# Kernel tuning notes

Hardware: AMD Instinct MI355X
Metric: run time of the kernel (lower is better)

Reference implementation:

```python
import jax, jax.numpy as jnp
import numpy as np

P = 16            # patch_size
D = 256           # hidden_dim == P*P (required by final reshape)
H = 8             # num_heads
HD = D // H       # head_dim


def _sinusoid(n, d):
    # standard sinusoidal positional encoding, interleaved sin/cos
    pos = jnp.arange(n, dtype=jnp.float32)[:, None]            # (n,1)
    i = jnp.arange(0, d, 2, dtype=jnp.float32)                 # (d/2,)
    div = jnp.exp(-i * (jnp.log(10000.0) / d))                 # (d/2,)
    ang = pos * div                                            # (n, d/2)
    return jnp.stack([jnp.sin(ang), jnp.cos(ang)], axis=-1).reshape(n, d)


def _patch_embed(x, w, b):
    # Conv2d(in_ch, D, kernel=P, stride=P) then flatten to (B, N, D)
    e = jax.lax.conv_general_dilated(
        x, w, window_strides=(P, P), padding='VALID',
        dimension_numbers=('NCHW', 'OIHW', 'NCHW'))
    e = e + b[None, :, None, None]
    B = e.shape[0]
    e = e.reshape(B, D, -1).transpose(0, 2, 1)                 # (B, N, D)
    e = e + _sinusoid(e.shape[1], D)[None]                     # positional enc
    return e.reshape(B, -1, H, HD).transpose(0, 2, 1, 3)       # (B, H, N, HD)


def setup_inputs() -> dict:
    key = jax.random.key(0)
    ks = jax.random.split(key, 12)
    B = 16
    inp = {
        'q': jax.random.normal(ks[0], (B, 3, 512, 512), jnp.float32),
        'k': jax.random.normal(ks[1], (B, 3, 512, 512), jnp.float32),
        'v': jax.random.normal(ks[2], (B, 3, 512, 512), jnp.float32),
        'a': jax.random.normal(ks[3], (B, 3, 256, 256), jnp.float32),
    }
    s = 0.02
    for idx, name in enumerate('qkva'):
        inp['w' + name] = jax.random.normal(ks[4 + 2 * idx], (D, 3, P, P), jnp.float32) * s
        inp['b' + name] = jnp.zeros((D,), jnp.float32)
    return inp


def reference(q, k, v, a, wq, bq, wk, bk, wv, bv, wa, ba):
    qh = _patch_embed(q, wq, bq)   # (B,H,Nq,HD), Nq=1024
    kh = _patch_embed(k, wk, bk)   # (B,H,Nk,HD)
    vh = _patch_embed(v, wv, bv)   # (B,H,Nk,HD)
    ah = _patch_embed(a, wa, ba)   # (B,H,Na,HD), Na=256
    scale = HD ** -0.5
    # agent attention: two small softmax matmuls then Q @ (K @ V)
    Qs = jax.nn.softmax(jnp.einsum('bhnd,bhmd->bhnm', qh, ah) * scale, axis=-1)  # (B,H,Nq,Na)
    Ks = jax.nn.softmax(jnp.einsum('bhmd,bhnd->bhmn', ah, kh) * scale, axis=-1)  # (B,H,Na,Nk)
    KV = jnp.einsum('bhmn,bhnd->bhmd', Ks, vh)                                   # (B,H,Na,HD)
    A = jnp.einsum('bhnm,bhmd->bhnd', Qs, KV)                                    # (B,H,Nq,HD)
    B = A.shape[0]
    attn = A.transpose(0, 2, 1, 3).reshape(B, -1, D)            # (B, Nq, D)
    N = attn.shape[1]
    g = int(N ** 0.5)                                           # grid side (32)
    HW = g * P                                                  # 512
    attn = attn.reshape(B, N, P, P)
    attn = attn.reshape(B, g, g, P, P).transpose(0, 1, 3, 2, 4).reshape(B, HW, HW)
    return attn
```

## Files before the change

### kernel.cpp

```cpp
#include <hip/hip_runtime.h>
#include <cstdint>
#include <cstddef>

typedef __bf16 bf16x8 __attribute__((ext_vector_type(8)));
typedef __bf16 bf16x4 __attribute__((ext_vector_type(4)));
typedef float f32x4 __attribute__((ext_vector_type(4)));
typedef unsigned short u16x4 __attribute__((ext_vector_type(4)));
typedef unsigned short u16x8 __attribute__((ext_vector_type(8)));

#define MFMA16(a, b, c) __builtin_amdgcn_mfma_f32_16x16x32_bf16(a, b, c, 0, 0, 0)

#define GLOAD16(g, l)                                                          \
    __builtin_amdgcn_global_load_lds(                                          \
        (const __attribute__((address_space(1))) unsigned int*)(g),            \
        (__attribute__((address_space(3))) unsigned int*)(l), 16, 0, 0)

__device__ __forceinline__ unsigned short f2bf(float f) {
    unsigned u = __builtin_bit_cast(unsigned, f);
    u = (u + 0x7FFFu + ((u >> 16) & 1u)) >> 16;
    return (unsigned short)u;
}

__global__ __launch_bounds__(256)
void prep(float* __restrict__ pe, float* __restrict__ peT, unsigned short* __restrict__ Wb,
          const float* __restrict__ w0, const float* __restrict__ w1,
          const float* __restrict__ w2, const float* __restrict__ w3) {
    const int bx = blockIdx.x, t = threadIdx.x;
    const float LC = 0.03597789207808881f;
    if (bx < 1024) {
        int n = bx, d = t;
        float div = expf(-(float)(2 * (d >> 1)) * LC);
        float ang = (float)n * div;
        pe[n * 256 + d] = (d & 1) ? cosf(ang) : sinf(ang);
    } else if (bx < 1280) {
        int d = bx - 1024;
        float div = expf(-(float)(2 * (d >> 1)) * LC);
        f32x4 o;
        int n0 = t * 4;
#pragma unroll
        for (int e = 0; e < 4; ++e) {
            float ang = (float)(n0 + e) * div;
            o[e] = (d & 1) ? cosf(ang) : sinf(ang);
        }
        *(f32x4*)&peT[(size_t)d * 1024 + n0] = o;
    } else {
        int i = bx - 1280;
        int tensor = i / 192, blk = i - tensor * 192;
        const float* w = (tensor == 0) ? w0 : (tensor == 1) ? w1 : (tensor == 2) ? w2 : w3;
        int idx4 = blk * 256 + t;
        int d = idx4 / 192;
        int kq4 = idx4 - d * 192;
        f32x4 v = *(const f32x4*)(w + (size_t)idx4 * 4);
        u16x4 o;
#pragma unroll
        for (int e = 0; e < 4; ++e) o[e] = f2bf(v[e]);
        int d16 = d & 15, kq_in = kq4 & 7;
        int slot = (kq_in >> 1) ^ ((d16 >> 1) & 3);
        unsigned short* dst = Wb + (size_t)tensor * 196608
                            + (d >> 4) * 12288 + (kq4 >> 3) * 512
                            + d16 * 32 + slot * 8 + (kq_in & 1) * 4;
        *(u16x4*)dst = o;
    }
}

struct EArgs {
    const float* src;
    const unsigned short* Wb;
    const float* bias;
    const float* pe;
    const float* peT;
    unsigned short* dst;
    int Np, lgNp, lgG, S, trans;
};

template<bool TR>
__device__ __forceinline__ void embed_body(const EArgs& A, int m0, int nh,
                                           float* Abuf0, float* Abuf1,
                                           unsigned short* Wbuf0, unsigned short* Wbuf1) {
    const int t = threadIdx.x, lane = t & 63, wid = t >> 6;
    const int l15 = lane & 15, l4 = lane >> 4;
    const int wr = wid >> 1, wc = wid & 1;
    const int S = A.S;
    const size_t S2 = (size_t)S * S;

    float* Ab[2] = { Abuf0, Abuf1 };
    unsigned short* Wbf[2] = { Wbuf0, Wbuf1 };

    const int kqL = (lane & 7) ^ (lane >> 3);
    const float* aP[2];
#pragma unroll
    for (int i = 0; i < 2; ++i) {
        int p = (wid * 2 + i) * 8 + (lane >> 3);
        int m = m0 + p;
        int b = m >> A.lgNp, n = m & (A.Np - 1);
        int gy = n >> A.lgG, gx = n & ((1 << A.lgG) - 1);
        aP[i] = A.src + ((size_t)(b * 3) * S + gy * 16 + (kqL >> 2)) * (size_t)S
              + gx * 16 + (kqL & 3) * 4;
    }
    const unsigned short* wP[2];
#pragma unroll
    for (int j = 0; j < 2; ++j)
        wP[j] = A.Wb + (size_t)(nh * 8 + wid * 2 + j) * 12288 + lane * 8;

    auto stage = [&](int kt, int buf) {
        size_t aoff = (size_t)(kt >> 3) * S2 + (size_t)((kt & 7) * 2) * S;
#pragma unroll
        for (int i = 0; i < 2; ++i)
            GLOAD16(aP[i] + aoff, Ab[buf] + (wid * 2 + i) * 256);
#pragma unroll
        for (int j = 0; j < 2; ++j)
            GLOAD16(wP[j] + kt * 512, Wbf[buf] + (wid * 2 + j) * 512);
    };

    f32x4 acc[2][4];
#pragma unroll
    for (int i = 0; i < 2; ++i)
#pragma unroll
        for (int j = 0; j < 4; ++j) acc[i][j] = f32x4{0.f, 0.f, 0.f, 0.f};

    auto compute = [&](int c) {
        bf16x8 pf[2];
#pragma unroll
        for (int i = 0; i < 2; ++i) {
            const char* base = (const char*)Ab[c] + (wr * 32 + i * 16 + l15) * 128;
            f32x4 lo = *(const f32x4*)(base + (((2 * l4) ^ (l15 & 7)) << 4));
            f32x4 hi = *(const f32x4*)(base + (((2 * l4 + 1) ^ (l15 & 7)) << 4));
            bf16x8 v;
#pragma unroll
            for (int e = 0; e < 4; ++e) { v[e] = (__bf16)lo[e]; v[4 + e] = (__bf16)hi[e]; }
            pf[i] = v;
        }
        bf16x8 wf[4];
#pragma unroll
        for (int j = 0; j < 4; ++j) {
            const char* base = (const char*)Wbf[c] + (wc * 4 + j) * 1024;
            u16x8 r = *(const u16x8*)(base + l15 * 64 + ((l4 ^ ((l15 >> 1) & 3)) << 4));
            wf[j] = __builtin_bit_cast(bf16x8, r);
        }
#pragma unroll
        for (int i = 0; i < 2; ++i)
#pragma unroll
            for (int j = 0; j < 4; ++j) {
                if (TR) acc[i][j] = MFMA16(pf[i], wf[j], acc[i][j]);
                else    acc[i][j] = MFMA16(wf[j], pf[i], acc[i][j]);
            }
    };

    stage(0, 0);
    stage(1, 1);

#pragma unroll 2
    for (int kt = 0; kt < 22; ++kt) {
        asm volatile("s_waitcnt vmcnt(4)" ::: "memory");
        __builtin_amdgcn_s_barrier();
        compute(kt & 1);
        asm volatile("s_waitcnt lgkmcnt(0)" ::: "memory");
        __builtin_amdgcn_sched_barrier(0);
        __builtin_amdgcn_s_barrier();
        stage(kt + 2, kt & 1);
    }
    asm volatile("s_waitcnt vmcnt(4)" ::: "memory");
    __builtin_amdgcn_s_barrier();
    compute(0);
    asm volatile("s_waitcnt lgkmcnt(0)" ::: "memory");
    __builtin_amdgcn_sched_barrier(0);
    __builtin_amdgcn_s_barrier();
    asm volatile("s_waitcnt vmcnt(0)" ::: "memory");
    __builtin_amdgcn_s_barrier();
    compute(1);

    if (!TR) {
#pragma unroll
        for (int j = 0; j < 4; ++j) {
            int d0 = nh * 128 + wc * 64 + j * 16 + l4 * 4;
            int hh = d0 >> 5, hd = d0 & 31;
            f32x4 bs = *(const f32x4*)&A.bias[d0];
#pragma unroll
            for (int i = 0; i < 2; ++i) {
                int p = m0 + wr * 32 + i * 16 + l15;
                int b = p >> A.lgNp, n = p & (A.Np - 1);
                f32x4 pv = *(const f32x4*)&A.pe[n * 256 + d0];
                bf16x4 o;
#pragma unroll
                for (int r = 0; r < 4; ++r)
                    o[r] = (__bf16)(acc[i][j][r] + bs[r] + pv[r]);
                *(bf16x4*)&A.dst[(((size_t)(b * 8 + hh)) * A.Np + n) * 32 + hd] = o;
            }
        }
    } else {
#pragma unroll
        for (int j = 0; j < 4; ++j) {
            int d = nh * 128 + wc * 64 + j * 16 + l15;
            int hh = d >> 5, hd = d & 31;
            float bsv = A.bias[d];
#pragma unroll
            for (int i = 0; i < 2; ++i) {
                int p0 = m0 + wr * 32 + i * 16 + l4 * 4;
                int b = p0 >> A.lgNp, n0 = p0 & (A.Np - 1);
                f32x4 pv = *(const f32x4*)&A.peT[(size_t)d * 1024 + n0];
                bf16x4 o;
#pragma unroll
                for (int r = 0; r < 4; ++r)
                    o[r] = (__bf16)(acc[i][j][r] + bsv + pv[r]);
                *(bf16x4*)&A.dst[(((size_t)(b * 8 + hh)) * 32 + hd) * (size_t)A.Np + n0] = o;
            }
        }
    }
}

__global__ __launch_bounds__(256, 4)
void embed5(EArgs A0, EArgs A1, EArgs A2, EArgs A3) {
    __shared__ float Abuf[2][2048];
    __shared__ unsigned short Wbuf[2][4096];
    const int bx = blockIdx.x;
    EArgs A; int lbx;
    if      (bx < 512)  { A = A0; lbx = bx; }
    else if (bx < 1024) { A = A1; lbx = bx - 512; }
    else if (bx < 1536) { A = A2; lbx = bx - 1024; }
    else                { A = A3; lbx = bx - 1536; }
    const int m0 = (lbx >> 1) * 64;
    const int nh = lbx & 1;
    if (A.trans) embed_body<true>(A, m0, nh, Abuf[0], Abuf[1], Wbuf[0], Wbuf[1]);
    else         embed_body<false>(A, m0, nh, Abuf[0], Abuf[1], Wbuf[0], Wbuf[1]);
}

__global__ __launch_bounds__(512)
void s2kv_kernel(const unsigned short* __restrict__ ah_ws,
                 const unsigned short* __restrict__ kh_ws,
                 const unsigned short* __restrict__ vT_ws,
                 unsigned short* __restrict__ kvT_ws) {
    __shared__ unsigned short ahs[128][40];
    __shared__ unsigned short khs[128][40];
    __shared__ unsigned short vts[32][136];
    __shared__ unsigned short Ps[128][136];

    const int bid = blockIdx.x;
    const int half = bid & 1;
    const int h = (bid >> 1) & 7, b = bid >> 4;
    const int a0 = half * 128;
    const int t = threadIdx.x, lane = t & 63, wid = t >> 6;
    const int l15 = lane & 15, l4 = lane >> 4;
    const size_t bh = (size_t)(b * 8 + h);

    const unsigned short* ahp = ah_ws + (bh * 256 + a0) * 32;
    const unsigned short* khp = kh_ws + bh * 1024 * 32;
    const unsigned short* vtp = vT_ws + bh * 32 * 1024;

    {
        int row = t >> 2, kq = (t & 3) * 8;
        *(u16x8*)&ahs[row][kq] = *(const u16x8*)(ahp + row * 32 + kq);
    }
    __syncthreads();
    const bf16x8 af = *(const bf16x8*)&ahs[wid * 16 + l15][l4 * 8];

    const float scale = 0.17677669529663687f;
    float rs[4] = {0.f, 0.f, 0.f, 0.f};
    const f32x4 z = {0.f, 0.f, 0.f, 0.f};
    f32x4 kv[2];
    kv[0] = z; kv[1] = z;

    for (int kt = 0; kt < 8; ++kt) {
        const int n0 = kt * 128;
        __syncthreads();
        {
            int row = t >> 2, kq = (t & 3) * 8;
            *(u16x8*)&khs[row][kq] = *(const u16x8*)(khp + (size_t)(n0 + row) * 32 + kq);
        }
        {
            int row = t >> 4, cq = (t & 15) * 8;
            *(u16x8*)&vts[row][cq] = *(const u16x8*)(vtp + (size_t)row * 1024 + n0 + cq);
        }
        __syncthreads();
#pragma unroll
        for (int n16 = 0; n16 < 8; ++n16) {
            bf16x8 bfr = *(const bf16x8*)&khs[n16 * 16 + l15][l4 * 8];
            f32x4 s = MFMA16(af, bfr, z);
#pragma unroll
            for (int r = 0; r < 4; ++r) {
                float e = __expf(s[r] * scale);
                rs[r] += e;
                Ps[wid * 16 + l4 * 4 + r][n16 * 16 + l15] = f2bf(e);
            }
        }
        __syncthreads();
#pragma unroll
        for (int ks = 0; ks < 4; ++ks) {
            bf16x8 pa = *(const bf16x8*)&Ps[wid * 16 + l15][ks * 32 + l4 * 8];
#pragma unroll
            for (int n16 = 0; n16 < 2; ++n16) {
                bf16x8 vb = *(const bf16x8*)&vts[n16 * 16 + l15][ks * 32 + l4 * 8];
                kv[n16] = MFMA16(pa, vb, kv[n16]);
            }
        }
    }
#pragma unroll
    for (int r = 0; r < 4; ++r) {
        rs[r] += __shfl_xor(rs[r], 1, 64);
        rs[r] += __shfl_xor(rs[r], 2, 64);
        rs[r] += __shfl_xor(rs[r], 4, 64);
        rs[r] += __shfl_xor(rs[r], 8, 64);
    }
#pragma unroll
    for (int n16 = 0; n16 < 2; ++n16)
#pragma unroll
        for (int r = 0; r < 4; ++r) {
            int m = a0 + wid * 16 + l4 * 4 + r;
            int d = n16 * 16 + l15;
            kvT_ws[bh * 8192 + (size_t)d * 256 + m] = f2bf(kv[n16][r] / rs[r]);
        }
}

__global__ __launch_bounds__(256)
void qsa_kernel(const unsigned short* __restrict__ qh_ws,
                const unsigned short* __restrict__ ah_ws,
                const unsigned short* __restrict__ kvT_ws,
                float* __restrict__ out) {
    __shared__ unsigned short qhs[64][40];
    __shared__ unsigned short ahs[256][40];
    __shared__ unsigned short kvt[32][264];
    __shared__ unsigned short Ps[64][264];

    const int bid = blockIdx.x;
    const int qt = bid & 15, h = (bid >> 4) & 7, b = bid >> 7;
    const int m0 = qt * 64;
    const int t = threadIdx.x, lane = t & 63, wid = t >> 6;
    const int l15 = lane & 15, l4 = lane >> 4;
    const size_t bh = (size_t)(b * 8 + h);

    const unsigned short* qhp = qh_ws + (bh * 1024 + m0) * 32;
    const unsigned short* ahp = ah_ws + bh * 256 * 32;

    {
        int row = t >> 2, kq = (t & 3) * 8;
        *(u16x8*)&qhs[row][kq] = *(const u16x8*)(qhp + row * 32 + kq);
    }
    {
        *(u16x8*)&ahs[t][0]  = *(const u16x8*)(ahp + (size_t)t * 32);
        *(u16x8*)&ahs[t][8]  = *(const u16x8*)(ahp + (size_t)t * 32 + 8);
        *(u16x8*)&ahs[t][16] = *(const u16x8*)(ahp + (size_t)t * 32 + 16);
        *(u16x8*)&ahs[t][24] = *(const u16x8*)(ahp + (size_t)t * 32 + 24);
    }
#pragma unroll
    for (int i = 0; i < 4; ++i) {
        int chunk = t + i * 256;
        int row = chunk >> 5, cq = (chunk & 31) * 8;
        *(u16x8*)&kvt[row][cq] = *(const u16x8*)(kvT_ws + bh * 8192 + (size_t)row * 256 + cq);
    }
    __syncthreads();

    const bf16x8 qa = *(const bf16x8*)&qhs[wid * 16 + l15][l4 * 8];
    const float scale = 0.17677669529663687f;
    const f32x4 z = {0.f, 0.f, 0.f, 0.f};
    float rs[4] = {0.f, 0.f, 0.f, 0.f};
#pragma unroll
    for (int n16 = 0; n16 < 16; ++n16) {
        bf16x8 bfr = *(const bf16x8*)&ahs[n16 * 16 + l15][l4 * 8];
        f32x4 s = MFMA16(qa, bfr, z);
#pragma unroll
        for (int r = 0; r < 4; ++r) {
            float e = __expf(s[r] * scale);
            rs[r] += e;
            Ps[wid * 16 + l4 * 4 + r][n16 * 16 + l15] = f2bf(e);
        }
    }
#pragma unroll
    for (int r = 0; r < 4; ++r) {
        rs[r] += __shfl_xor(rs[r], 1, 64);
        rs[r] += __shfl_xor(rs[r], 2, 64);
        rs[r] += __shfl_xor(rs[r], 4, 64);
        rs[r] += __shfl_xor(rs[r], 8, 64);
    }
    __syncthreads();

    f32x4 o[2];
    o[0] = z; o[1] = z;
#pragma unroll
    for (int ks = 0; ks < 8; ++ks) {
        bf16x8 pa = *(const bf16x8*)&Ps[wid * 16 + l15][ks * 32 + l4 * 8];
#pragma unroll
        for (int n16 = 0; n16 < 2; ++n16) {
            bf16x8 kb = *(const bf16x8*)&kvt[n16 * 16 + l15][ks * 32 + l4 * 8];
            o[n16] = MFMA16(pa, kb, o[n16]);
        }
    }
#pragma unroll
    for (int n16 = 0; n16 < 2; ++n16) {
#pragma unroll
        for (int r = 0; r < 4; ++r) {
            int row = wid * 16 + l4 * 4 + r;
            int n = m0 + row;
            int gy = n >> 5, gx = n & 31;
            int hd = n16 * 16 + l15;
            int py = 2 * h + (hd >> 4), px = hd & 15;
            out[((size_t)b * 512 + gy * 16 + py) * 512 + gx * 16 + px] = o[n16][r] / rs[r];
        }
    }
}

extern "C" void kernel_launch(void* const* d_in, const int* in_sizes, int n_in,
                              void* d_out, int out_size, void* d_ws, size_t ws_size,
                              hipStream_t stream) {
    (void)in_sizes; (void)n_in; (void)out_size; (void)ws_size;

    const float* q  = (const float*)d_in[0];
    const float* k  = (const float*)d_in[1];
    const float* v  = (const float*)d_in[2];
    const float* a  = (const float*)d_in[3];
    const float* wq = (const float*)d_in[4];
    const float* bq = (const float*)d_in[5];
    const float* wk = (const float*)d_in[6];
    const float* bk = (const float*)d_in[7];
    const float* wv = (const float*)d_in[8];
    const float* bv = (const float*)d_in[9];
    const float* wa = (const float*)d_in[10];
    const float* ba = (const float*)d_in[11];
    float* out = (float*)d_out;

    char* ws = (char*)d_ws;
    float* pe           = (float*)(ws);
    float* peT          = (float*)(ws + 1048576);
    unsigned short* Wb  = (unsigned short*)(ws + 2097152);
    unsigned short* kvT = (unsigned short*)(ws);
    unsigned short* qh  = (unsigned short*)(ws + 3670016);
    unsigned short* kh  = (unsigned short*)(ws + 12058624);
    unsigned short* ah  = (unsigned short*)(ws + 20447232);
    unsigned short* vT  = (unsigned short*)(ws + 22544384);

    prep<<<2048, 256, 0, stream>>>(pe, peT, Wb, wq, wk, wv, wa);

    EArgs Aq = { q, Wb,              bq, pe, peT, qh, 1024, 10, 5, 512, 0 };
    EArgs Ak = { k, Wb + 196608,     bk, pe, peT, kh, 1024, 10, 5, 512, 0 };
    EArgs Av = { v, Wb + 2 * 196608, bv, pe, peT, vT, 1024, 10, 5, 512, 1 };
    EArgs Aa = { a, Wb + 3 * 196608, ba, pe, peT, ah,  256,  8, 4, 256, 0 };
    embed5<<<1664, 256, 0, stream>>>(Aq, Ak, Av, Aa);

    s2kv_kernel<<<256, 512, 0, stream>>>(ah, kh, vT, kvT);
    qsa_kernel<<<2048, 256, 0, stream>>>(qh, ah, kvT, out);
}
```

Before: 106.3 us.

## Load conv weights directly into registers and triple-buffer activation tiles

The patch-embed GEMM now reads the pre-packed bf16 weight fragments straight from global memory into registers, double-buffered across iterations, instead of staging them through LDS. The prep kernel's weight layout drops its bank swizzle to match this per-lane read pattern. The activation tiles in LDS go from two buffers to three, so each iteration needs only one barrier instead of two. In exchange each wave issues more global traffic for weights (redundant across waves sharing wc) and holds more registers.

```diff
diff --git a/kernel.cpp b/kernel.cpp
--- a/kernel.cpp
+++ b/kernel.cpp
@@ -49,16 +49,14 @@
         const float* w = (tensor == 0) ? w0 : (tensor == 1) ? w1 : (tensor == 2) ? w2 : w3;
         int idx4 = blk * 256 + t;
         int d = idx4 / 192;
-        int kq4 = idx4 - d * 192;
+        int kq = (idx4 - d * 192) * 4;
         f32x4 v = *(const f32x4*)(w + (size_t)idx4 * 4);
         u16x4 o;
 #pragma unroll
         for (int e = 0; e < 4; ++e) o[e] = f2bf(v[e]);
-        int d16 = d & 15, kq_in = kq4 & 7;
-        int slot = (kq_in >> 1) ^ ((d16 >> 1) & 3);
         unsigned short* dst = Wb + (size_t)tensor * 196608
-                            + (d >> 4) * 12288 + (kq4 >> 3) * 512
-                            + d16 * 32 + slot * 8 + (kq_in & 1) * 4;
+                            + (d >> 4) * 12288 + (kq >> 5) * 512
+                            + (d & 15) * 32 + (kq & 31);
         *(u16x4*)dst = o;
     }
 }
@@ -74,17 +72,12 @@
 };
 
 template<bool TR>
-__device__ __forceinline__ void embed_body(const EArgs& A, int m0, int nh,
-                                           float* Abuf0, float* Abuf1,
-                                           unsigned short* Wbuf0, unsigned short* Wbuf1) {
+__device__ __forceinline__ void embed_body(const EArgs& A, int m0, int nh, float* Abuf) {
     const int t = threadIdx.x, lane = t & 63, wid = t >> 6;
     const int l15 = lane & 15, l4 = lane >> 4;
     const int wr = wid >> 1, wc = wid & 1;
     const int S = A.S;
     const size_t S2 = (size_t)S * S;
-
-    float* Ab[2] = { Abuf0, Abuf1 };
-    unsigned short* Wbf[2] = { Wbuf0, Wbuf1 };
 
     const int kqL = (lane & 7) ^ (lane >> 3);
     const float* aP[2];
@@ -97,20 +90,22 @@
         aP[i] = A.src + ((size_t)(b * 3) * S + gy * 16 + (kqL >> 2)) * (size_t)S
               + gx * 16 + (kqL & 3) * 4;
     }
-    const unsigned short* wP[2];
-#pragma unroll
-    for (int j = 0; j < 2; ++j)
-        wP[j] = A.Wb + (size_t)(nh * 8 + wid * 2 + j) * 12288 + lane * 8;
-
-    auto stage = [&](int kt, int buf) {
-        size_t aoff = (size_t)(kt >> 3) * S2 + (size_t)((kt & 7) * 2) * S;
+    const unsigned short* wbase = A.Wb + (size_t)(nh * 8 + wc * 4) * 12288
+                                + l15 * 32 + l4 * 8;
+
+    auto stageA = [&](int kt, int slot) {
+        size_t aoff = (size_t)(kt >> 3) * S2 + (size_t)((kt & 7) * 2) * (size_t)S;
 #pragma unroll
         for (int i = 0; i < 2; ++i)
-            GLOAD16(aP[i] + aoff, Ab[buf] + (wid * 2 + i) * 256);
-#pragma unroll
-        for (int j = 0; j < 2; ++j)
-            GLOAD16(wP[j] + kt * 512, Wbf[buf] + (wid * 2 + j) * 512);
+            GLOAD16(aP[i] + aoff, Abuf + slot * 2048 + (wid * 2 + i) * 256);
     };
+    auto loadW = [&](int kt, bf16x8* w) {
+#pragma unroll
+        for (int j = 0; j < 4; ++j) {
+            u16x8 r = *(const u16x8*)(wbase + (size_t)j * 12288 + kt * 512);
+            w[j] = __builtin_bit_cast(bf16x8, r);
+        }
+    };
 
     f32x4 acc[2][4];
 #pragma unroll
@@ -118,24 +113,20 @@
 #pragma unroll
         for (int j = 0; j < 4; ++j) acc[i][j] = f32x4{0.f, 0.f, 0.f, 0.f};
 
-    auto compute = [&](int c) {
+    bf16x8 wpf[2][4];
+
+    auto compute = [&](int slot, const bf16x8* wf) {
         bf16x8 pf[2];
 #pragma unroll
         for (int i = 0; i < 2; ++i) {
-            const char* base = (const char*)Ab[c] + (wr * 32 + i * 16 + l15) * 128;
+            const char* base = (const char*)(Abuf + slot * 2048)
+                             + (wr * 32 + i * 16 + l15) * 128;
             f32x4 lo = *(const f32x4*)(base + (((2 * l4) ^ (l15 & 7)) << 4));
             f32x4 hi = *(const f32x4*)(base + (((2 * l4 + 1) ^ (l15 & 7)) << 4));
             bf16x8 v;
 #pragma unroll
             for (int e = 0; e < 4; ++e) { v[e] = (__bf16)lo[e]; v[4 + e] = (__bf16)hi[e]; }
             pf[i] = v;
-        }
-        bf16x8 wf[4];
-#pragma unroll
-        for (int j = 0; j < 4; ++j) {
-            const char* base = (const char*)Wbf[c] + (wc * 4 + j) * 1024;
-            u16x8 r = *(const u16x8*)(base + l15 * 64 + ((l4 ^ ((l15 >> 1) & 3)) << 4));
-            wf[j] = __builtin_bit_cast(bf16x8, r);
         }
 #pragma unroll
         for (int i = 0; i < 2; ++i)
@@ -146,33 +137,36 @@
             }
     };
 
-    stage(0, 0);
-    stage(1, 1);
-
-#pragma unroll 2
+    stageA(0, 0);
+    stageA(1, 1);
+    loadW(0, wpf[0]);
+    loadW(1, wpf[1]);
+
+#pragma unroll 6
     for (int kt = 0; kt < 22; ++kt) {
-        asm volatile("s_waitcnt vmcnt(4)" ::: "memory");
-        __builtin_amdgcn_s_barrier();
-        compute(kt & 1);
+        asm volatile("s_waitcnt vmcnt(6)" ::: "memory");
         asm volatile("s_waitcnt lgkmcnt(0)" ::: "memory");
         __builtin_amdgcn_sched_barrier(0);
         __builtin_amdgcn_s_barrier();
-        stage(kt + 2, kt & 1);
-    }
-    asm volatile("s_waitcnt vmcnt(4)" ::: "memory");
-    __builtin_amdgcn_s_barrier();
-    compute(0);
+        compute(kt % 3, wpf[kt & 1]);
+        stageA(kt + 2, (kt + 2) % 3);
+        loadW(kt + 2, wpf[kt & 1]);
+    }
+    asm volatile("s_waitcnt vmcnt(6)" ::: "memory");
     asm volatile("s_waitcnt lgkmcnt(0)" ::: "memory");
     __builtin_amdgcn_sched_barrier(0);
     __builtin_amdgcn_s_barrier();
+    compute(22 % 3, wpf[0]);
     asm volatile("s_waitcnt vmcnt(0)" ::: "memory");
+    asm volatile("s_waitcnt lgkmcnt(0)" ::: "memory");
+    __builtin_amdgcn_sched_barrier(0);
     __builtin_amdgcn_s_barrier();
-    compute(1);
+    compute(23 % 3, wpf[1]);
 
     if (!TR) {
 #pragma unroll
         for (int j = 0; j < 4; ++j) {
-            int d0 = nh * 128 + wc * 64 + j * 16 + l4 * 4;
+            int d0 = (nh * 8 + wc * 4 + j) * 16 + l4 * 4;
             int hh = d0 >> 5, hd = d0 & 31;
             f32x4 bs = *(const f32x4*)&A.bias[d0];
 #pragma unroll
@@ -190,7 +184,7 @@
     } else {
 #pragma unroll
         for (int j = 0; j < 4; ++j) {
-            int d = nh * 128 + wc * 64 + j * 16 + l15;
+            int d = (nh * 8 + wc * 4 + j) * 16 + l15;
             int hh = d >> 5, hd = d & 31;
             float bsv = A.bias[d];
 #pragma unroll
@@ -209,9 +203,8 @@
 }
 
 __global__ __launch_bounds__(256, 4)
-void embed5(EArgs A0, EArgs A1, EArgs A2, EArgs A3) {
-    __shared__ float Abuf[2][2048];
-    __shared__ unsigned short Wbuf[2][4096];
+void embed8(EArgs A0, EArgs A1, EArgs A2, EArgs A3) {
+    __shared__ float Abuf[3][2048];
     const int bx = blockIdx.x;
     EArgs A; int lbx;
     if      (bx < 512)  { A = A0; lbx = bx; }
@@ -220,8 +213,8 @@
     else                { A = A3; lbx = bx - 1536; }
     const int m0 = (lbx >> 1) * 64;
     const int nh = lbx & 1;
-    if (A.trans) embed_body<true>(A, m0, nh, Abuf[0], Abuf[1], Wbuf[0], Wbuf[1]);
-    else         embed_body<false>(A, m0, nh, Abuf[0], Abuf[1], Wbuf[0], Wbuf[1]);
+    if (A.trans) embed_body<true>(A, m0, nh, &Abuf[0][0]);
+    else         embed_body<false>(A, m0, nh, &Abuf[0][0]);
 }
 
 __global__ __launch_bounds__(512)
@@ -432,7 +425,7 @@
     EArgs Ak = { k, Wb + 196608,     bk, pe, peT, kh, 1024, 10, 5, 512, 0 };
     EArgs Av = { v, Wb + 2 * 196608, bv, pe, peT, vT, 1024, 10, 5, 512, 1 };
     EArgs Aa = { a, Wb + 3 * 196608, ba, pe, peT, ah,  256,  8, 4, 256, 0 };
-    embed5<<<1664, 256, 0, stream>>>(Aq, Ak, Av, Aa);
+    embed8<<<1664, 256, 0, stream>>>(Aq, Ak, Av, Aa);
 
     s2kv_kernel<<<256, 512, 0, stream>>>(ah, kh, vT, kvT);
     qsa_kernel<<<2048, 256, 0, stream>>>(qh, ah, kvT, out);
```

Result: slower. 108.9 us (+2.4%).
